# Kernel optimization log

Measured on AMD Instinct MI355X. Metric: run time of the kernel, lower is better.

Reference implementation:

```python
import jax, jax.numpy as jnp
import numpy as np

DIMS = 256; K = 3; G = 4; CG = DIMS // G; P = K * K
STRIDE = 1; PAD = K // 2; DIL = 1; OFFSET_SCALE = 1.0; SOFTMAX = False
PW_OUT = int(np.ceil(G * P * 3 / 8) * 8)  # 112


def setup_inputs() -> dict:
    key = jax.random.key(0)
    ks = jax.random.split(key, 6)
    N, H, W = 4, 64, 64
    x = jax.random.normal(ks[0], (N, DIMS, H, W), dtype=jnp.float32)
    dw_w = jax.random.normal(ks[1], (DIMS, 1, K, K), dtype=jnp.float32) * 0.1
    dw_b = jnp.zeros((DIMS,), dtype=jnp.float32)
    pw_w = jax.random.normal(ks[2], (PW_OUT, DIMS), dtype=jnp.float32) * 0.01
    pw_b = jnp.zeros((PW_OUT,), dtype=jnp.float32)
    pin_w = jax.random.normal(ks[3], (DIMS, DIMS), dtype=jnp.float32) * (1.0 / np.sqrt(DIMS))
    pin_b = jnp.zeros((DIMS,), dtype=jnp.float32)
    pout_w = jax.random.normal(ks[4], (DIMS, DIMS), dtype=jnp.float32) * (1.0 / np.sqrt(DIMS))
    pout_b = jnp.zeros((DIMS,), dtype=jnp.float32)
    return {"x": x, "dw_w": dw_w, "dw_b": dw_b, "pw_w": pw_w, "pw_b": pw_b,
            "pin_w": pin_w, "pin_b": pin_b, "pout_w": pout_w, "pout_b": pout_b}


def _forward(x, dw_w, dw_b, pw_w, pw_b, pin_w, pin_b, pout_w, pout_b):
    N, C, H, W = x.shape
    L = H * W
    inp = x.reshape(N, C, L).transpose(0, 2, 1)              # [N, L, C]
    # input projection
    val = inp @ pin_w.T + pin_b                               # [N, L, C]
    # offset/mask head: depthwise conv (on raw input) + pointwise linear
    om = jax.lax.conv_general_dilated(
        x, dw_w, window_strides=(1, 1), padding=[(PAD, PAD), (PAD, PAD)],
        dimension_numbers=("NCHW", "OIHW", "NCHW"), feature_group_count=C)
    om = om + dw_b[None, :, None, None]
    om = om.reshape(N, C, L).transpose(0, 2, 1)               # [N, L, C]
    om = om @ pw_w.T + pw_b                                   # [N, L, PW_OUT]
    om = om[..., : G * P * 3].reshape(N, L, G, P, 3)
    off_x = om[..., 0] * OFFSET_SCALE                         # [N, L, G, P]
    off_y = om[..., 1] * OFFSET_SCALE
    mask = om[..., 2]
    if SOFTMAX:
        mask = jax.nn.softmax(mask, axis=-1)
    # kernel grid (P points)
    ky, kx = jnp.meshgrid(jnp.arange(K), jnp.arange(K), indexing="ij")
    ky = (ky.reshape(-1) * DIL).astype(jnp.float32)           # [P]
    kx = (kx.reshape(-1) * DIL).astype(jnp.float32)
    # base output positions (stride 1, zero pad)
    yb = jnp.repeat(jnp.arange(H), W).astype(jnp.float32) * STRIDE - PAD   # [L]
    xb = jnp.tile(jnp.arange(W), H).astype(jnp.float32) * STRIDE - PAD
    pos_y = yb[None, :, None, None] + ky[None, None, None, :] + off_y     # [N,L,G,P]
    pos_x = xb[None, :, None, None] + kx[None, None, None, :] + off_x
    # bilinear gather from grouped value tensor
    vflat = val.reshape(N * L * G, CG)
    n_ids = jnp.arange(N)[:, None, None, None]
    g_ids = jnp.arange(G)[None, None, :, None]

    def gather(iy, ix):
        valid = (iy >= 0) & (iy < H) & (ix >= 0) & (ix < W)
        sidx = jnp.clip(iy, 0, H - 1) * W + jnp.clip(ix, 0, W - 1)
        gidx = (n_ids * L + sidx) * G + g_ids                 # [N,L,G,P]
        v = vflat[gidx]                                       # [N,L,G,P,CG]
        return jnp.where(valid[..., None], v, 0.0)

    y0 = jnp.floor(pos_y); x0 = jnp.floor(pos_x)
    fy = pos_y - y0; fx = pos_x - x0
    iy0 = y0.astype(jnp.int32); ix0 = x0.astype(jnp.int32)
    iy1 = iy0 + 1; ix1 = ix0 + 1
    w00 = (1 - fy) * (1 - fx); w01 = (1 - fy) * fx
    w10 = fy * (1 - fx); w11 = fy * fx
    acc = (jnp.einsum("nlgp,nlgpc->nlgc", mask * w00, gather(iy0, ix0))
           + jnp.einsum("nlgp,nlgpc->nlgc", mask * w01, gather(iy0, ix1))
           + jnp.einsum("nlgp,nlgpc->nlgc", mask * w10, gather(iy1, ix0))
           + jnp.einsum("nlgp,nlgpc->nlgc", mask * w11, gather(iy1, ix1)))
    out = acc.reshape(N, L, C)
    out = out @ pout_w.T + pout_b                             # output projection
    return out.transpose(0, 2, 1).reshape(N, C, H, W)


def reference(x, dw_w, dw_b, pw_w, pw_b, pin_w, pin_b, pout_w, pout_b):
    return _forward(x, dw_w, dw_b, pw_w, pw_b, pin_w, pin_b, pout_w, pout_b)
```

## Files before the change

kernel.cpp:

```cpp
#include <hip/hip_runtime.h>

typedef unsigned short u16;
typedef short bf16x8 __attribute__((ext_vector_type(8)));
typedef u16 u16x8 __attribute__((ext_vector_type(8)));
typedef float f32x4 __attribute__((ext_vector_type(4)));

#define K_DIM 256
#define L_DIM 4096
#define NBATCH 4

static __device__ __forceinline__ u16 f2bf(float f) {
    unsigned u = __float_as_uint(f);
    unsigned r = (u + 0x7FFFu + ((u >> 16) & 1u)) >> 16;
    return (u16)r;
}
static __device__ __forceinline__ float bf2f(u16 v) {
    return __uint_as_float(((unsigned)v) << 16);
}

#define GLOAD16(g, l) __builtin_amdgcn_global_load_lds( \
    (const __attribute__((address_space(1))) void*)(g), \
    (__attribute__((address_space(3))) void*)(l), 16, 0, 0)

__global__ __launch_bounds__(256) void prep_kernel(
    const float* __restrict__ x, const float* __restrict__ dw_w,
    const float* __restrict__ dw_b, const float* __restrict__ pin_w,
    const float* __restrict__ pw_w, const float* __restrict__ pout_w,
    u16* __restrict__ xb_t, u16* __restrict__ dwc_t,
    u16* __restrict__ pin_wb, u16* __restrict__ pw_wb,
    u16* __restrict__ pout_wb)
{
    if (blockIdx.x == 4) {
        if (blockIdx.z != 0) return;
        const int end = (blockIdx.y + 1) * 2560;
        for (int k = blockIdx.y * 2560 + threadIdx.x; k < end; k += 256) {
            if (k < 65536) pin_wb[k] = f2bf(pin_w[k]);
            else if (k < 98304) {
                int j = k - 65536;
                pw_wb[j] = ((j >> 8) < 112) ? f2bf(pw_w[j]) : (u16)0;
            } else {
                int j = k - 98304;
                pout_wb[j] = f2bf(pout_w[j]);
            }
        }
        return;
    }

    __shared__ u16 tx_[64][66];
    __shared__ u16 td_[64][66];
    const int c0 = blockIdx.x * 64, h = blockIdx.y, n = blockIdx.z;
    const int t = threadIdx.x;
    const float* xn = x + (size_t)n * 256 * L_DIM;

    const int w4 = (t & 15) * 4;
    const int cs = t >> 4;

    #pragma unroll
    for (int j = 0; j < 4; ++j) {
        const int cl = cs * 4 + j, c = c0 + cl;
        const float* xc = xn + (size_t)c * L_DIM;
        const float* w9 = dw_w + c * 9;

        float s[4];
        const float bv = dw_b[c];
        #pragma unroll
        for (int k = 0; k < 4; ++k) s[k] = bv;
        f32x4 center;

        #pragma unroll
        for (int dy = 0; dy < 3; ++dy) {
            const int hh = h + dy - 1;
            if (hh < 0 || hh > 63) continue;
            const float* row = xc + hh * 64;
            const f32x4 m = *(const f32x4*)(row + w4);
            const float flv = row[(w4 > 0) ? w4 - 1 : 0];
            const float frv = row[(w4 + 4 < 64) ? w4 + 4 : 63];
            if (dy == 1) center = m;
            #pragma unroll
            for (int k = 0; k < 4; ++k) {
                const int w = w4 + k;
                const float lv = (w > 0) ? 1.f : 0.f;
                const float rv = (w < 63) ? 1.f : 0.f;
                const float xm = (k == 0) ? flv : m[k - 1];
                const float xp = (k == 3) ? frv : m[k + 1];
                s[k] = fmaf(xm * lv, w9[dy*3 + 0], s[k]);
                s[k] = fmaf(m[k],    w9[dy*3 + 1], s[k]);
                s[k] = fmaf(xp * rv, w9[dy*3 + 2], s[k]);
            }
        }
        #pragma unroll
        for (int k = 0; k < 4; ++k) {
            tx_[w4 + k][cl] = f2bf(center[k]);
            td_[w4 + k][cl] = f2bf(s[k]);
        }
    }
    __syncthreads();

    const int cc = t & 63, cq = t >> 6;
    for (int j = 0; j < 16; ++j) {
        const int wl = j * 4 + cq;
        const size_t o = ((size_t)n * L_DIM + h * 64 + wl) * 256 + c0 + cc;
        xb_t[o]  = tx_[wl][cc];
        dwc_t[o] = td_[wl][cc];
    }
}

__global__ __launch_bounds__(256) void gemm_dual(
    const u16* __restrict__ xb_t, const u16* __restrict__ dwc_t,
    const u16* __restrict__ pin_wb, const u16* __restrict__ pw_wb,
    const float* __restrict__ pin_b, const float* __restrict__ pw_b,
    u16* __restrict__ val_b, float* __restrict__ omb)
{
    __shared__ u16 lds[16384];
    const int bx = blockIdx.x;
    const bool isPw = (bx == 2);
    const u16* Ag = isPw ? dwc_t : xb_t;
    const u16* Bg = isPw ? pw_wb : pin_wb;
    const float* bias = isPw ? pw_b : pin_b;
    const int n0 = isPw ? 0 : bx * 128;
    const int Ncols = isPw ? 112 : 256;
    const int ldC = isPw ? 112 : 256;
    const int m0 = blockIdx.y * 128;

    const int t = threadIdx.x;
    const int wave = t >> 6, lane = t & 63;
    const int lr = lane & 15, lk = lane >> 4;
    const int wr = wave >> 1, wc = wave & 1;
    const int wbase = wave << 10;

    const int srow = t >> 2;
    const int scol = (t & 3) * 8;
    const u16* ga0 = Ag + (size_t)(m0 + srow)      * K_DIM + scol;
    const u16* ga1 = Ag + (size_t)(m0 + 64 + srow) * K_DIM + scol;
    const u16* gb0 = Bg + (size_t)(n0 + srow)      * K_DIM + scol;
    const u16* gb1 = Bg + (size_t)(n0 + 64 + srow) * K_DIM + scol;

    f32x4 acc[4][4];
    #pragma unroll
    for (int m = 0; m < 4; ++m)
        #pragma unroll
        for (int n = 0; n < 4; ++n) acc[m][n] = (f32x4){0.f, 0.f, 0.f, 0.f};

    auto stage = [&](int b, int kt) {
        const int ko = kt * 32;
        char* base = (char*)lds + b * 16384 + wbase;
        GLOAD16(ga0 + ko, base);
        GLOAD16(ga1 + ko, base + 4096);
        GLOAD16(gb0 + ko, base + 8192);
        GLOAD16(gb1 + ko, base + 12288);
    };

    stage(0, 0);
    asm volatile("s_waitcnt vmcnt(0)" ::: "memory");
    __syncthreads();

    for (int kt = 0; kt < 8; ++kt) {
        const int cur = kt & 1;
        if (kt < 7) stage(cur ^ 1, kt + 1);
        const char* la = (const char*)lds + cur * 16384;
        const char* lb = la + 8192;
        bf16x8 af[4], bfr[4];
        #pragma unroll
        for (int m = 0; m < 4; ++m)
            af[m] = *(const bf16x8*)(la + ((wr*64 + m*16 + lr) * 32 + lk * 8) * 2);
        #pragma unroll
        for (int n = 0; n < 4; ++n)
            bfr[n] = *(const bf16x8*)(lb + ((wc*64 + n*16 + lr) * 32 + lk * 8) * 2);
        #pragma unroll
        for (int m = 0; m < 4; ++m)
            #pragma unroll
            for (int n = 0; n < 4; ++n)
                acc[m][n] = __builtin_amdgcn_mfma_f32_16x16x32_bf16(
                    af[m], bfr[n], acc[m][n], 0, 0, 0);
        asm volatile("s_waitcnt vmcnt(0)" ::: "memory");
        __syncthreads();
    }

    #pragma unroll
    for (int m = 0; m < 4; ++m) {
        #pragma unroll
        for (int n = 0; n < 4; ++n) {
            const int col = n0 + wc*64 + n*16 + lr;
            if (col < Ncols) {
                const float bv = bias[col];
                #pragma unroll
                for (int r = 0; r < 4; ++r) {
                    const int row = m0 + wr*64 + m*16 + lk*4 + r;
                    const float o = acc[m][n][r] + bv;
                    const size_t off = (size_t)row * ldC + col;
                    if (isPw) omb[off] = o;
                    else      val_b[off] = f2bf(o);
                }
            }
        }
    }
}

__global__ __launch_bounds__(256, 4) void gather_kernel(
    const float* __restrict__ om, const u16* __restrict__ val,
    u16* __restrict__ accb)
{
    __shared__ float som[904];
    const int blk = blockIdx.x;
    const int grp = (blk & 7) * 256 + (blk >> 3);
    const int n = grp >> 9;
    const int l0 = (grp & 511) * 8;
    const int t = threadIdx.x;

    {
        const float* omsrc = om + ((size_t)n * L_DIM + l0) * 112;
        if (t < 224) {
            const int wb = (t >> 6) << 10;
            GLOAD16(omsrc + t * 4, (char*)som + wb);
        }
        asm volatile("s_waitcnt vmcnt(0)" ::: "memory");
        __syncthreads();
    }

    const int pos = t >> 5;
    const int g = (t >> 3) & 3;
    const int ch = (t & 7) * 8;
    const int l = l0 + pos;
    const float* omp = som + pos * 112 + g * 27;
    const u16* vb = val + (size_t)n * L_DIM * 256 + g * 64 + ch;
    const float ybase = (float)(l >> 6) - 1.f;
    const float xb = (float)(l & 63) - 1.f;

    float a[8];
    #pragma unroll
    for (int j = 0; j < 8; ++j) a[j] = 0.f;

    #pragma unroll
    for (int p = 0; p < 9; ++p) {
        const float ox = omp[p*3 + 0];
        const float oy = omp[p*3 + 1];
        const float mk = omp[p*3 + 2];
        const float py = ybase + (float)(p / 3) + oy;
        const float px = xb + (float)(p % 3) + ox;
        const float y0 = floorf(py), x0 = floorf(px);
        const float fy = py - y0, fx = px - x0;
        const int iy0 = (int)y0, ix0 = (int)x0;
        const float wy[2] = {mk * (1.f - fy), mk * fy};
        const float wx[2] = {1.f - fx, fx};
        #pragma unroll
        for (int c4 = 0; c4 < 4; ++c4) {
            const int dy = c4 >> 1, dx = c4 & 1;
            const int iy = iy0 + dy, ix = ix0 + dx;
            const bool ok = ((unsigned)iy < 64u) & ((unsigned)ix < 64u);
            const float wgt = ok ? wy[dy] * wx[dx] : 0.f;
            const int iyc = min(max(iy, 0), 63);
            const int ixc = min(max(ix, 0), 63);
            const u16x8 v = *(const u16x8*)(vb + (size_t)(iyc * 64 + ixc) * 256);
            #pragma unroll
            for (int j = 0; j < 8; ++j) a[j] = fmaf(wgt, bf2f(v[j]), a[j]);
        }
    }
    u16x8 o;
    #pragma unroll
    for (int j = 0; j < 8; ++j) o[j] = f2bf(a[j]);
    *(u16x8*)(accb + ((size_t)n * L_DIM + l) * 256 + g * 64 + ch) = o;
}

__global__ __launch_bounds__(256) void gemm_pout(
    const u16* __restrict__ accb, const u16* __restrict__ pout_wb,
    const float* __restrict__ pout_b, float* __restrict__ out)
{
    __shared__ u16 lds[16384];
    const int z = blockIdx.z;
    const u16* Bg = accb + (size_t)z * L_DIM * 256;
    const int n0 = blockIdx.x * 128;
    const int m0 = blockIdx.y * 128;

    const int t = threadIdx.x;
    const int wave = t >> 6, lane = t & 63;
    const int lr = lane & 15, lk = lane >> 4;
    const int wr = wave >> 1, wc = wave & 1;
    const int wbase = wave << 10;

    const int srow = t >> 2;
    const int scol = (t & 3) * 8;
    const u16* ga0 = pout_wb + (size_t)(m0 + srow)      * K_DIM + scol;
    const u16* ga1 = pout_wb + (size_t)(m0 + 64 + srow) * K_DIM + scol;
    const u16* gb0 = Bg + (size_t)(n0 + srow)      * K_DIM + scol;
    const u16* gb1 = Bg + (size_t)(n0 + 64 + srow) * K_DIM + scol;

    f32x4 acc[4][4];
    #pragma unroll
    for (int m = 0; m < 4; ++m)
        #pragma unroll
        for (int n = 0; n < 4; ++n) acc[m][n] = (f32x4){0.f, 0.f, 0.f, 0.f};

    auto stage = [&](int b, int kt) {
        const int ko = kt * 32;
        char* base = (char*)lds + b * 16384 + wbase;
        GLOAD16(ga0 + ko, base);
        GLOAD16(ga1 + ko, base + 4096);
        GLOAD16(gb0 + ko, base + 8192);
        GLOAD16(gb1 + ko, base + 12288);
    };

    stage(0, 0);
    asm volatile("s_waitcnt vmcnt(0)" ::: "memory");
    __syncthreads();

    for (int kt = 0; kt < 8; ++kt) {
        const int cur = kt & 1;
        if (kt < 7) stage(cur ^ 1, kt + 1);
        const char* la = (const char*)lds + cur * 16384;
        const char* lb = la + 8192;
        bf16x8 af[4], bfr[4];
        #pragma unroll
        for (int m = 0; m < 4; ++m)
            af[m] = *(const bf16x8*)(la + ((wr*64 + m*16 + lr) * 32 + lk * 8) * 2);
        #pragma unroll
        for (int n = 0; n < 4; ++n)
            bfr[n] = *(const bf16x8*)(lb + ((wc*64 + n*16 + lr) * 32 + lk * 8) * 2);
        #pragma unroll
        for (int m = 0; m < 4; ++m)
            #pragma unroll
            for (int n = 0; n < 4; ++n)
                acc[m][n] = __builtin_amdgcn_mfma_f32_16x16x32_bf16(
                    af[m], bfr[n], acc[m][n], 0, 0, 0);
        asm volatile("s_waitcnt vmcnt(0)" ::: "memory");
        __syncthreads();
    }

    float* outn = out + (size_t)z * 256 * L_DIM;
    #pragma unroll
    for (int m = 0; m < 4; ++m) {
        #pragma unroll
        for (int n = 0; n < 4; ++n) {
            const int col = n0 + wc*64 + n*16 + lr;
            #pragma unroll
            for (int r = 0; r < 4; ++r) {
                const int row = m0 + wr*64 + m*16 + lk*4 + r;
                outn[(size_t)row * L_DIM + col] = acc[m][n][r] + pout_b[row];
            }
        }
    }
}

extern "C" void kernel_launch(void* const* d_in, const int* in_sizes, int n_in,
                              void* d_out, int out_size, void* d_ws, size_t ws_size,
                              hipStream_t stream) {
    const float* x      = (const float*)d_in[0];
    const float* dw_w   = (const float*)d_in[1];
    const float* dw_b   = (const float*)d_in[2];
    const float* pw_w   = (const float*)d_in[3];
    const float* pw_b   = (const float*)d_in[4];
    const float* pin_w  = (const float*)d_in[5];
    const float* pin_b  = (const float*)d_in[6];
    const float* pout_w = (const float*)d_in[7];
    const float* pout_b = (const float*)d_in[8];
    float* out = (float*)d_out;

    char* ws = (char*)d_ws;
    u16*   xb_t    = (u16*)ws;
    u16*   dwc_t   = (u16*)(ws + 8388608);
    u16*   val_b   = (u16*)(ws + 16777216);
    u16*   acc_b   = (u16*)(ws + 25165824);
    float* omb     = (float*)(ws + 33554432);
    u16*   pin_wb  = (u16*)(ws + 40894464);
    u16*   pw_wb   = (u16*)(ws + 41025536);
    u16*   pout_wb = (u16*)(ws + 41091072);

    prep_kernel<<<dim3(5, 64, NBATCH), 256, 0, stream>>>(
        x, dw_w, dw_b, pin_w, pw_w, pout_w,
        xb_t, dwc_t, pin_wb, pw_wb, pout_wb);

    gemm_dual<<<dim3(3, 128), 256, 0, stream>>>(
        xb_t, dwc_t, pin_wb, pw_wb, pin_b, pw_b, val_b, omb);

    gather_kernel<<<dim3(2048), 256, 0, stream>>>(omb, val_b, acc_b);

    gemm_pout<<<dim3(32, 2, NBATCH), 256, 0, stream>>>(
        acc_b, pout_wb, pout_b, out);
}
```

Baseline: 57.46 us.

## Double-buffer gather loads via global_load_lds staging in deformable sampling kernel

Replaces direct global vector loads of the four bilinear corner values with asynchronous global-to-LDS copies into a two-deep staging buffer, issuing loads for sampling point p+2 while computing point p. The goal is to hide gather latency behind arithmetic in a latency-bound kernel. It adds 32KB of LDS per block, which may cut occupancy below the 4 blocks per CU the launch bounds request. It also recomputes the sampling coordinates for the issue step.

```diff
diff --git a/kernel.cpp b/kernel.cpp
--- a/kernel.cpp
+++ b/kernel.cpp
@@ -201,6 +201,7 @@
     u16* __restrict__ accb)
 {
     __shared__ float som[904];
+    __shared__ u16 stage[2][4][2048];
     const int blk = blockIdx.x;
     const int grp = (blk & 7) * 256 + (blk >> 3);
     const int n = grp >> 9;
@@ -226,14 +227,42 @@
     const float ybase = (float)(l >> 6) - 1.f;
     const float xb = (float)(l & 63) - 1.f;
 
+    auto ISSUE = [&](int p, int buf) {
+        const float oy = omp[p*3 + 1];
+        const float ox = omp[p*3 + 0];
+        const float py = ybase + (float)(p / 3) + oy;
+        const float px = xb + (float)(p % 3) + ox;
+        const int iy0 = (int)floorf(py);
+        const int ix0 = (int)floorf(px);
+        #pragma unroll
+        for (int c4 = 0; c4 < 4; ++c4) {
+            const int iy = iy0 + (c4 >> 1), ix = ix0 + (c4 & 1);
+            const int iyc = min(max(iy, 0), 63);
+            const int ixc = min(max(ix, 0), 63);
+            GLOAD16(vb + (size_t)(iyc * 64 + ixc) * 256, &stage[buf][c4][t * 8]);
+        }
+    };
+
     float a[8];
     #pragma unroll
     for (int j = 0; j < 8; ++j) a[j] = 0.f;
 
+    ISSUE(0, 0);
+    ISSUE(1, 1);
+
     #pragma unroll
     for (int p = 0; p < 9; ++p) {
+        const int buf = p & 1;
+        if (p < 8) { asm volatile("s_waitcnt vmcnt(4)" ::: "memory"); }
+        else       { asm volatile("s_waitcnt vmcnt(0)" ::: "memory"); }
+        const u16x8 v0 = *(const u16x8*)&stage[buf][0][t * 8];
+        const u16x8 v1 = *(const u16x8*)&stage[buf][1][t * 8];
+        const u16x8 v2 = *(const u16x8*)&stage[buf][2][t * 8];
+        const u16x8 v3 = *(const u16x8*)&stage[buf][3][t * 8];
+        asm volatile("s_waitcnt lgkmcnt(0)" ::: "memory");
+        if (p < 7) ISSUE(p + 2, buf);
+        const float oy = omp[p*3 + 1];
         const float ox = omp[p*3 + 0];
-        const float oy = omp[p*3 + 1];
         const float mk = omp[p*3 + 2];
         const float py = ybase + (float)(p / 3) + oy;
         const float px = xb + (float)(p % 3) + ox;
@@ -242,19 +271,23 @@
         const int iy0 = (int)y0, ix0 = (int)x0;
         const float wy[2] = {mk * (1.f - fy), mk * fy};
         const float wx[2] = {1.f - fx, fx};
+        float wgt[4];
         #pragma unroll
         for (int c4 = 0; c4 < 4; ++c4) {
-            const int dy = c4 >> 1, dx = c4 & 1;
-            const int iy = iy0 + dy, ix = ix0 + dx;
+            const int iy = iy0 + (c4 >> 1), ix = ix0 + (c4 & 1);
             const bool ok = ((unsigned)iy < 64u) & ((unsigned)ix < 64u);
-            const float wgt = ok ? wy[dy] * wx[dx] : 0.f;
-            const int iyc = min(max(iy, 0), 63);
-            const int ixc = min(max(ix, 0), 63);
-            const u16x8 v = *(const u16x8*)(vb + (size_t)(iyc * 64 + ixc) * 256);
-            #pragma unroll
-            for (int j = 0; j < 8; ++j) a[j] = fmaf(wgt, bf2f(v[j]), a[j]);
-        }
-    }
+            wgt[c4] = ok ? wy[c4 >> 1] * wx[c4 & 1] : 0.f;
+        }
+        #pragma unroll
+        for (int j = 0; j < 8; ++j) a[j] = fmaf(wgt[0], bf2f(v0[j]), a[j]);
+        #pragma unroll
+        for (int j = 0; j < 8; ++j) a[j] = fmaf(wgt[1], bf2f(v1[j]), a[j]);
+        #pragma unroll
+        for (int j = 0; j < 8; ++j) a[j] = fmaf(wgt[2], bf2f(v2[j]), a[j]);
+        #pragma unroll
+        for (int j = 0; j < 8; ++j) a[j] = fmaf(wgt[3], bf2f(v3[j]), a[j]);
+    }
+
     u16x8 o;
     #pragma unroll
     for (int j = 0; j < 8; ++j) o[j] = f2bf(a[j]);
```

New measurement: 213.7 us. 272% more time.
